# Performance work log

Hardware: AMD Instinct MI355X
Metric: run time of the kernel (lower is better)

Reference implementation:

```python
import jax, jax.numpy as jnp
import numpy as np

EPS = 1e-3  # Keras LayerNormalization default epsilon


def setup_inputs() -> dict:
    key = jax.random.key(0)
    ks = jax.random.split(key, 10)
    B, S, D, U = 4, 4096, 1024, 1024
    sc_in = 1.0 / np.sqrt(D)
    sc_u = 1.0 / np.sqrt(U)
    return {
        "inputs": jax.random.normal(ks[0], (B, S, D), dtype=jnp.float32),
        "w1": jax.random.normal(ks[1], (D, U), dtype=jnp.float32) * sc_in,
        "b1": jnp.zeros((U,), dtype=jnp.float32),
        "w2": jax.random.normal(ks[2], (U, U), dtype=jnp.float32) * sc_u,
        "b2": jnp.zeros((U,), dtype=jnp.float32),
        "wg": jax.random.normal(ks[3], (D, U), dtype=jnp.float32) * sc_in,
        "bg": jnp.zeros((U,), dtype=jnp.float32),
        "ws": jax.random.normal(ks[4], (D, U), dtype=jnp.float32) * sc_in,
        "bs": jnp.zeros((U,), dtype=jnp.float32),
        "gamma": jnp.ones((U,), dtype=jnp.float32),
        "beta": jnp.zeros((U,), dtype=jnp.float32),
    }


def reference(inputs, w1, b1, w2, b2, wg, bg, ws, bs, gamma, beta):
    # hidden branch: Dense(relu) -> (dropout inactive at inference) -> Dense
    h = jax.nn.relu(jnp.einsum('bsd,du->bsu', inputs, w1) + b1)
    x = jnp.einsum('bsu,uv->bsv', h, w2) + b2
    # gate on raw inputs
    g = jax.nn.sigmoid(jnp.einsum('bsd,du->bsu', inputs, wg) + bg)
    # skip projection
    s = jnp.einsum('bsd,du->bsu', inputs, ws) + bs
    y = x * g + s
    # LayerNormalization over last axis (Keras default eps=1e-3)
    mu = jnp.mean(y, axis=-1, keepdims=True)
    var = jnp.mean(jnp.square(y - mu), axis=-1, keepdims=True)
    return (y - mu) * jax.lax.rsqrt(var + EPS) * gamma + beta
```

## Files before the change

kernel.cpp:

```cpp
#include <hip/hip_runtime.h>
#include <hip/hip_bf16.h>

typedef short short8 __attribute__((ext_vector_type(8)));
typedef float f32x4 __attribute__((ext_vector_type(4)));

#define M_TOT 16384
#define NDIM  1024
#define BM 256
#define BN 256
#define BK 32
#define NT (NDIM / BK)

static __device__ __forceinline__ unsigned short f2bf(float f) {
  unsigned int u = __builtin_bit_cast(unsigned int, f);
  unsigned int r = (u + 0x7fffu + ((u >> 16) & 1u)) >> 16;
  return (unsigned short)r;
}
static __device__ __forceinline__ float bf2f(unsigned short u) {
  return __builtin_bit_cast(float, ((unsigned int)u) << 16);
}

#define CLB() asm volatile("" ::: "memory")

__global__ __launch_bounds__(256) void cast_in(const float* __restrict__ in,
                                               unsigned short* __restrict__ out,
                                               int n4) {
  int i = blockIdx.x * 256 + threadIdx.x;
  if (i >= n4) return;
  float4 v = reinterpret_cast<const float4*>(in)[i];
  ushort4 o;
  o.x = f2bf(v.x); o.y = f2bf(v.y); o.z = f2bf(v.z); o.w = f2bf(v.w);
  reinterpret_cast<ushort4*>(out)[i] = o;
}

__global__ __launch_bounds__(256) void tcast(const float* __restrict__ src,
                                             unsigned short* __restrict__ dst) {
  __shared__ unsigned short tile[32][33];
  int bx = blockIdx.x * 32, by = blockIdx.y * 32;
  int x = threadIdx.x & 31, y = threadIdx.x >> 5;
#pragma unroll
  for (int i = 0; i < 32; i += 8)
    tile[y + i][x] = f2bf(src[(size_t)(by + y + i) * NDIM + bx + x]);
  __syncthreads();
#pragma unroll
  for (int i = 0; i < 32; i += 8)
    dst[(size_t)(bx + y + i) * NDIM + by + x] = tile[x][y + i];
}

template <int MODE>
__global__ __launch_bounds__(512, 2) void gemm256(
    const unsigned short* __restrict__ A,
    const unsigned short* __restrict__ Bt,
    const float* __restrict__ bias,
    unsigned short* __restrict__ O,
    const unsigned short* __restrict__ G,
    const unsigned short* __restrict__ S) {
  __shared__ __align__(16) unsigned short lds[4][2][256][BK];

  const int tid = threadIdx.x;
  const int lane = tid & 63;
  const int wave = tid >> 6;
  const int wm = wave >> 2;
  const int wn = wave & 3;

  const int id = blockIdx.x;
  const int xcd = id & 7;
  const int slot0 = id >> 3;
  const int rblk = xcd + 8 * (slot0 >> 2);
  const int cblk = slot0 & 3;
  const int m0 = rblk * BM, n0 = cblk * BN;

  const unsigned short* gA = A + (size_t)m0 * NDIM;
  const unsigned short* gB = Bt + (size_t)n0 * NDIM;

  f32x4 acc[8][4] = {};

  auto stage = [&](int slot, int kt) {
#pragma unroll
    for (int q = 0; q < 4; ++q) {
      int cid = q * 512 + tid;
      int mat = q >> 1;
      int local = cid & 1023;
      int row = local >> 2;
      int c = (local & 3) ^ ((row >> 1) & 3);
      const unsigned short* g =
          (mat ? gB : gA) + (size_t)row * NDIM + kt * BK + c * 8;
      unsigned short* l = &lds[slot][mat][0][0] +
                          (size_t)((q * 512 + (tid & ~63)) & 1023) * 8;
      __builtin_amdgcn_global_load_lds(
          (__attribute__((address_space(1))) void*)g,
          (__attribute__((address_space(3))) void*)l, 16, 0, 0);
    }
  };

  auto compute = [&](int slot) {
    short8 af[8], bf[4];
#pragma unroll
    for (int nj = 0; nj < 4; ++nj) {
      int row = wn * 64 + nj * 16 + (lane & 15);
      int cs = (lane >> 4) ^ ((row >> 1) & 3);
      bf[nj] = *reinterpret_cast<const short8*>(&lds[slot][1][row][cs * 8]);
    }
#pragma unroll
    for (int mi = 0; mi < 8; ++mi) {
      int row = wm * 128 + mi * 16 + (lane & 15);
      int cs = (lane >> 4) ^ ((row >> 1) & 3);
      af[mi] = *reinterpret_cast<const short8*>(&lds[slot][0][row][cs * 8]);
    }
    __builtin_amdgcn_s_setprio(1);
#pragma unroll
    for (int mi = 0; mi < 8; ++mi)
#pragma unroll
      for (int nj = 0; nj < 4; ++nj)
        acc[mi][nj] = __builtin_amdgcn_mfma_f32_16x16x32_bf16(
            af[mi], bf[nj], acc[mi][nj], 0, 0, 0);
    __builtin_amdgcn_s_setprio(0);
  };

#define VMW(N) asm volatile("s_waitcnt vmcnt(" #N ")" ::: "memory")
#define BAR() do { CLB(); __builtin_amdgcn_s_barrier(); CLB(); } while (0)

  stage(0, 0);
  stage(1, 1);
  stage(2, 2);
  VMW(8);
  BAR();

#pragma unroll 4
  for (int t = 0; t < NT - 4; ++t) {
    stage((t + 3) & 3, t + 3);
    compute(t & 3);
    VMW(8);
    BAR();
  }
  stage(3, 31);
  compute(0);
  VMW(8);
  BAR();
  compute(1);
  VMW(4);
  BAR();
  compute(2);
  VMW(0);
  BAR();
  compute(3);

  const int crow0 = m0 + wm * 128;
  const int ccol0 = n0 + wn * 64;
#pragma unroll
  for (int mi = 0; mi < 8; ++mi) {
#pragma unroll
    for (int nj = 0; nj < 4; ++nj) {
      int row = crow0 + mi * 16 + ((lane >> 4) << 2);
      int col = ccol0 + nj * 16 + (lane & 15);
      float bc = bias[col];
#pragma unroll
      for (int r = 0; r < 4; ++r) {
        float v = acc[mi][nj][r] + bc;
        size_t idx = (size_t)(row + r) * NDIM + col;
        if (MODE == 0) {
          O[idx] = f2bf(fmaxf(v, 0.f));
        } else if (MODE == 1) {
          O[idx] = f2bf(1.f / (1.f + __expf(-v)));
        } else if (MODE == 2) {
          O[idx] = f2bf(v);
        } else {
          O[idx] = f2bf(v * bf2f(G[idx]) + bf2f(S[idx]));
        }
      }
    }
  }
#undef VMW
#undef BAR
}

__global__ __launch_bounds__(256) void layernorm_bf(
    const unsigned short* __restrict__ Ybf, float* __restrict__ Out,
    const float* __restrict__ gamma, const float* __restrict__ beta) {
  const int tid = threadIdx.x;
  const unsigned short* y = Ybf + (size_t)blockIdx.x * NDIM;
  ushort4 u = reinterpret_cast<const ushort4*>(y)[tid];
  float v0 = bf2f(u.x), v1 = bf2f(u.y), v2 = bf2f(u.z), v3 = bf2f(u.w);
  float s1 = v0 + v1 + v2 + v3;
  float s2 = v0 * v0 + v1 * v1 + v2 * v2 + v3 * v3;
#pragma unroll
  for (int o = 32; o > 0; o >>= 1) {
    s1 += __shfl_down(s1, o, 64);
    s2 += __shfl_down(s2, o, 64);
  }
  __shared__ float red[8];
  int wave = tid >> 6, lane = tid & 63;
  if (lane == 0) { red[wave] = s1; red[wave + 4] = s2; }
  __syncthreads();
  float S1 = red[0] + red[1] + red[2] + red[3];
  float S2 = red[4] + red[5] + red[6] + red[7];
  float mu = S1 * (1.f / NDIM);
  float var = S2 * (1.f / NDIM) - mu * mu;
  float inv = rsqrtf(var + 1e-3f);
  float4 gm = reinterpret_cast<const float4*>(gamma)[tid];
  float4 bt = reinterpret_cast<const float4*>(beta)[tid];
  float4 o;
  o.x = (v0 - mu) * inv * gm.x + bt.x;
  o.y = (v1 - mu) * inv * gm.y + bt.y;
  o.z = (v2 - mu) * inv * gm.z + bt.z;
  o.w = (v3 - mu) * inv * gm.w + bt.w;
  reinterpret_cast<float4*>(Out + (size_t)blockIdx.x * NDIM)[tid] = o;
}

extern "C" void kernel_launch(void* const* d_in, const int* in_sizes, int n_in,
                              void* d_out, int out_size, void* d_ws, size_t ws_size,
                              hipStream_t stream) {
  const float* inp = (const float*)d_in[0];
  const float* w1 = (const float*)d_in[1];
  const float* b1 = (const float*)d_in[2];
  const float* w2 = (const float*)d_in[3];
  const float* b2 = (const float*)d_in[4];
  const float* wg = (const float*)d_in[5];
  const float* bg = (const float*)d_in[6];
  const float* wsk = (const float*)d_in[7];
  const float* bs = (const float*)d_in[8];
  const float* gamma = (const float*)d_in[9];
  const float* beta = (const float*)d_in[10];

  char* p = (char*)d_ws;
  const size_t act_bf16 = (size_t)M_TOT * NDIM * 2;
  const size_t w_bf16 = (size_t)NDIM * NDIM * 2;
  unsigned short* Ain = (unsigned short*)p; p += act_bf16;
  unsigned short* H   = (unsigned short*)p; p += act_bf16;
  unsigned short* G   = (unsigned short*)p; p += act_bf16;
  unsigned short* S   = (unsigned short*)p; p += act_bf16;
  unsigned short* Ybf = (unsigned short*)p; p += act_bf16;
  unsigned short* W1t = (unsigned short*)p; p += w_bf16;
  unsigned short* W2t = (unsigned short*)p; p += w_bf16;
  unsigned short* Wgt = (unsigned short*)p; p += w_bf16;
  unsigned short* Wst = (unsigned short*)p; p += w_bf16;

  cast_in<<<(M_TOT * NDIM / 4 + 255) / 256, 256, 0, stream>>>(inp, Ain, M_TOT * NDIM / 4);
  dim3 tg(32, 32);
  tcast<<<tg, 256, 0, stream>>>(w1, W1t);
  tcast<<<tg, 256, 0, stream>>>(w2, W2t);
  tcast<<<tg, 256, 0, stream>>>(wg, Wgt);
  tcast<<<tg, 256, 0, stream>>>(wsk, Wst);

  const int nblk = (M_TOT / BM) * (NDIM / BN);
  gemm256<0><<<nblk, 512, 0, stream>>>(Ain, W1t, b1, H, nullptr, nullptr);
  gemm256<1><<<nblk, 512, 0, stream>>>(Ain, Wgt, bg, G, nullptr, nullptr);
  gemm256<2><<<nblk, 512, 0, stream>>>(Ain, Wst, bs, S, nullptr, nullptr);
  gemm256<3><<<nblk, 512, 0, stream>>>(H, W2t, b2, Ybf, G, S);
  layernorm_bf<<<M_TOT, 256, 0, stream>>>(Ybf, (float*)d_out, gamma, beta);
}
```

Measured before the change: 201.6 us.

## Fuse the three input-projection GEMMs into one kernel sharing the A tile

Replaces three separate GEMM launches over the input (W1, gate, skip) with one kernel. Each 128x128 block loads the A tile once and multiplies it against all three weight tiles, writing relu, sigmoid and linear outputs from the epilogue. This cuts repeated loads of the input activations and two kernel launches. In exchange it uses a simpler double-buffered pipeline with two barriers per step, smaller tiles, and 192 accumulator registers per thread, which raises register pressure.

```diff
diff --git a/kernel.cpp b/kernel.cpp
--- a/kernel.cpp
+++ b/kernel.cpp
@@ -6,8 +6,6 @@
 
 #define M_TOT 16384
 #define NDIM  1024
-#define BM 256
-#define BN 256
 #define BK 32
 #define NT (NDIM / BK)
 
@@ -21,6 +19,8 @@
 }
 
 #define CLB() asm volatile("" ::: "memory")
+#define VMW(N) asm volatile("s_waitcnt vmcnt(" #N ")" ::: "memory")
+#define BAR() do { CLB(); __builtin_amdgcn_s_barrier(); CLB(); } while (0)
 
 __global__ __launch_bounds__(256) void cast_in(const float* __restrict__ in,
                                                unsigned short* __restrict__ out,
@@ -47,8 +47,123 @@
     dst[(size_t)(bx + y + i) * NDIM + by + x] = tile[x][y + i];
 }
 
-template <int MODE>
-__global__ __launch_bounds__(512, 2) void gemm256(
+__global__ __launch_bounds__(256, 2) void trigemm(
+    const unsigned short* __restrict__ A,
+    const unsigned short* __restrict__ W1t,
+    const unsigned short* __restrict__ Wgt,
+    const unsigned short* __restrict__ Wst,
+    const float* __restrict__ b1,
+    const float* __restrict__ bg,
+    const float* __restrict__ bs,
+    unsigned short* __restrict__ H,
+    unsigned short* __restrict__ G,
+    unsigned short* __restrict__ S) {
+  __shared__ __align__(16) unsigned short lds[2][4][128][BK];
+
+  const int tid = threadIdx.x;
+  const int lane = tid & 63;
+  const int wave = tid >> 6;
+  const int wm = wave >> 1;
+  const int wn = wave & 1;
+
+  const int id = blockIdx.x;
+  const int xcd = id & 7;
+  const int slot = id >> 3;
+  const int rblk = xcd + 8 * (slot >> 3);
+  const int cblk = slot & 7;
+  const int m0 = rblk * 128, n0 = cblk * 128;
+
+  const unsigned short* gA = A + (size_t)m0 * NDIM;
+  const unsigned short* gW[3] = {W1t + (size_t)n0 * NDIM, Wgt + (size_t)n0 * NDIM,
+                                 Wst + (size_t)n0 * NDIM};
+
+  f32x4 acc[3][4][4] = {};
+
+  auto stage = [&](int buf, int kt) {
+#pragma unroll
+    for (int q = 0; q < 8; ++q) {
+      const int mat = q >> 1;
+      int local = (q & 1) * 256 + tid;
+      int row = local >> 2;
+      int c = (local & 3) ^ ((row >> 1) & 3);
+      const unsigned short* g =
+          (mat == 0 ? gA : gW[mat - 1]) + (size_t)row * NDIM + kt * BK + c * 8;
+      unsigned short* l = &lds[buf][0][0][0] +
+                          (size_t)(q * 256 + (tid & ~63)) * 8;
+      __builtin_amdgcn_global_load_lds(
+          (__attribute__((address_space(1))) void*)g,
+          (__attribute__((address_space(3))) void*)l, 16, 0, 0);
+    }
+  };
+
+  auto compute = [&](int buf) {
+    short8 af[4];
+#pragma unroll
+    for (int mi = 0; mi < 4; ++mi) {
+      int row = wm * 64 + mi * 16 + (lane & 15);
+      int cs = (lane >> 4) ^ ((row >> 1) & 3);
+      af[mi] = *reinterpret_cast<const short8*>(&lds[buf][0][row][cs * 8]);
+    }
+#pragma unroll
+    for (int w = 0; w < 3; ++w) {
+      short8 bf[4];
+#pragma unroll
+      for (int nj = 0; nj < 4; ++nj) {
+        int row = wn * 64 + nj * 16 + (lane & 15);
+        int cs = (lane >> 4) ^ ((row >> 1) & 3);
+        bf[nj] = *reinterpret_cast<const short8*>(&lds[buf][1 + w][row][cs * 8]);
+      }
+      __builtin_amdgcn_s_setprio(1);
+#pragma unroll
+      for (int mi = 0; mi < 4; ++mi)
+#pragma unroll
+        for (int nj = 0; nj < 4; ++nj)
+          acc[w][mi][nj] = __builtin_amdgcn_mfma_f32_16x16x32_bf16(
+              af[mi], bf[nj], acc[w][mi][nj], 0, 0, 0);
+      __builtin_amdgcn_s_setprio(0);
+    }
+  };
+
+  stage(0, 0);
+  for (int t = 0; t < NT; ++t) {
+    const int cur = t & 1;
+    if (t + 1 < NT) {
+      stage(cur ^ 1, t + 1);
+      VMW(8);
+    } else {
+      VMW(0);
+    }
+    BAR();
+    compute(cur);
+    BAR();
+  }
+
+  const int crow0 = m0 + wm * 64;
+  const int ccol0 = n0 + wn * 64;
+#pragma unroll
+  for (int w = 0; w < 3; ++w) {
+    const float* bptr = (w == 0) ? b1 : (w == 1) ? bg : bs;
+    unsigned short* optr = (w == 0) ? H : (w == 1) ? G : S;
+#pragma unroll
+    for (int mi = 0; mi < 4; ++mi) {
+#pragma unroll
+      for (int nj = 0; nj < 4; ++nj) {
+        int row = crow0 + mi * 16 + ((lane >> 4) << 2);
+        int col = ccol0 + nj * 16 + (lane & 15);
+        float bc = bptr[col];
+#pragma unroll
+        for (int r = 0; r < 4; ++r) {
+          float v = acc[w][mi][nj][r] + bc;
+          if (w == 0) v = fmaxf(v, 0.f);
+          else if (w == 1) v = 1.f / (1.f + __expf(-v));
+          optr[(size_t)(row + r) * NDIM + col] = f2bf(v);
+        }
+      }
+    }
+  }
+}
+
+__global__ __launch_bounds__(512, 2) void gemm_y(
     const unsigned short* __restrict__ A,
     const unsigned short* __restrict__ Bt,
     const float* __restrict__ bias,
@@ -68,7 +183,7 @@
   const int slot0 = id >> 3;
   const int rblk = xcd + 8 * (slot0 >> 2);
   const int cblk = slot0 & 3;
-  const int m0 = rblk * BM, n0 = cblk * BN;
+  const int m0 = rblk * 256, n0 = cblk * 256;
 
   const unsigned short* gA = A + (size_t)m0 * NDIM;
   const unsigned short* gB = Bt + (size_t)n0 * NDIM;
@@ -117,9 +232,6 @@
     __builtin_amdgcn_s_setprio(0);
   };
 
-#define VMW(N) asm volatile("s_waitcnt vmcnt(" #N ")" ::: "memory")
-#define BAR() do { CLB(); __builtin_amdgcn_s_barrier(); CLB(); } while (0)
-
   stage(0, 0);
   stage(1, 1);
   stage(2, 2);
@@ -158,20 +270,10 @@
       for (int r = 0; r < 4; ++r) {
         float v = acc[mi][nj][r] + bc;
         size_t idx = (size_t)(row + r) * NDIM + col;
-        if (MODE == 0) {
-          O[idx] = f2bf(fmaxf(v, 0.f));
-        } else if (MODE == 1) {
-          O[idx] = f2bf(1.f / (1.f + __expf(-v)));
-        } else if (MODE == 2) {
-          O[idx] = f2bf(v);
-        } else {
-          O[idx] = f2bf(v * bf2f(G[idx]) + bf2f(S[idx]));
-        }
+        O[idx] = f2bf(v * bf2f(G[idx]) + bf2f(S[idx]));
       }
     }
   }
-#undef VMW
-#undef BAR
 }
 
 __global__ __launch_bounds__(256) void layernorm_bf(
@@ -242,10 +344,8 @@
   tcast<<<tg, 256, 0, stream>>>(wg, Wgt);
   tcast<<<tg, 256, 0, stream>>>(wsk, Wst);
 
-  const int nblk = (M_TOT / BM) * (NDIM / BN);
-  gemm256<0><<<nblk, 512, 0, stream>>>(Ain, W1t, b1, H, nullptr, nullptr);
-  gemm256<1><<<nblk, 512, 0, stream>>>(Ain, Wgt, bg, G, nullptr, nullptr);
-  gemm256<2><<<nblk, 512, 0, stream>>>(Ain, Wst, bs, S, nullptr, nullptr);
-  gemm256<3><<<nblk, 512, 0, stream>>>(H, W2t, b2, Ybf, G, S);
+  trigemm<<<(M_TOT / 128) * (NDIM / 128), 256, 0, stream>>>(
+      Ain, W1t, Wgt, Wst, b1, bg, bs, H, G, S);
+  gemm_y<<<(M_TOT / 256) * (NDIM / 256), 512, 0, stream>>>(H, W2t, b2, Ybf, G, S);
   layernorm_bf<<<M_TOT, 256, 0, stream>>>(Ybf, (float*)d_out, gamma, beta);
 }
```

New measurement: 195.2 us. -3.2%, faster.

## Restructure GEMM into 8-phase ping-pong pipeline with BK=64 half-tile staging

Applied to the files above, without the earlier changes.

Replaces the 4-slot BK=32 GEMM main loop with a double-buffered BK=64 scheme. Each tile is split into 128-row halves that are staged one at a time, interleaved with quarter-tile MFMA blocks across eight barrier-separated phases. LDS swizzling changes to an 8-chunk XOR pattern. The four weight transpose-cast launches are also merged into one kernel with a z-dimension. The goal is finer overlap of global-to-LDS loads with MFMA work and fewer loop iterations, at the cost of many more barriers per iteration.

```diff
diff --git a/kernel.cpp b/kernel.cpp
--- a/kernel.cpp
+++ b/kernel.cpp
@@ -6,10 +6,8 @@
 
 #define M_TOT 16384
 #define NDIM  1024
-#define BM 256
-#define BN 256
-#define BK 32
-#define NT (NDIM / BK)
+#define BK 64
+#define NI (NDIM / (2 * BK))
 
 static __device__ __forceinline__ unsigned short f2bf(float f) {
   unsigned int u = __builtin_bit_cast(unsigned int, f);
@@ -21,6 +19,9 @@
 }
 
 #define CLB() asm volatile("" ::: "memory")
+#define VMW(N) asm volatile("s_waitcnt vmcnt(" #N ")" ::: "memory")
+#define LGKM0() asm volatile("s_waitcnt lgkmcnt(0)" ::: "memory")
+#define BAR() do { CLB(); __builtin_amdgcn_s_barrier(); CLB(); } while (0)
 
 __global__ __launch_bounds__(256) void cast_in(const float* __restrict__ in,
                                                unsigned short* __restrict__ out,
@@ -33,8 +34,14 @@
   reinterpret_cast<ushort4*>(out)[i] = o;
 }
 
-__global__ __launch_bounds__(256) void tcast(const float* __restrict__ src,
-                                             unsigned short* __restrict__ dst) {
+__global__ __launch_bounds__(256) void tcast4(
+    const float* __restrict__ w1, const float* __restrict__ w2,
+    const float* __restrict__ wg, const float* __restrict__ ws,
+    unsigned short* __restrict__ W1t, unsigned short* __restrict__ W2t,
+    unsigned short* __restrict__ Wgt, unsigned short* __restrict__ Wst) {
+  const int z = blockIdx.z;
+  const float* src = (z == 0) ? w1 : (z == 1) ? w2 : (z == 2) ? wg : ws;
+  unsigned short* dst = (z == 0) ? W1t : (z == 1) ? W2t : (z == 2) ? Wgt : Wst;
   __shared__ unsigned short tile[32][33];
   int bx = blockIdx.x * 32, by = blockIdx.y * 32;
   int x = threadIdx.x & 31, y = threadIdx.x >> 5;
@@ -48,102 +55,152 @@
 }
 
 template <int MODE>
-__global__ __launch_bounds__(512, 2) void gemm256(
+__global__ __launch_bounds__(512, 2) void gemm8p(
     const unsigned short* __restrict__ A,
     const unsigned short* __restrict__ Bt,
     const float* __restrict__ bias,
     unsigned short* __restrict__ O,
     const unsigned short* __restrict__ G,
     const unsigned short* __restrict__ S) {
-  __shared__ __align__(16) unsigned short lds[4][2][256][BK];
+  __shared__ __align__(16) unsigned short lds[2][2][2][128][64];
 
   const int tid = threadIdx.x;
   const int lane = tid & 63;
   const int wave = tid >> 6;
   const int wm = wave >> 2;
   const int wn = wave & 3;
+  const int lr = lane & 15;
+  const int lk = lane >> 4;
 
   const int id = blockIdx.x;
   const int xcd = id & 7;
-  const int slot0 = id >> 3;
-  const int rblk = xcd + 8 * (slot0 >> 2);
-  const int cblk = slot0 & 3;
-  const int m0 = rblk * BM, n0 = cblk * BN;
+  const int slot = id >> 3;
+  const int rblk = xcd + 8 * (slot >> 2);
+  const int cblk = slot & 3;
+  const int m0 = rblk * 256, n0 = cblk * 256;
 
   const unsigned short* gA = A + (size_t)m0 * NDIM;
   const unsigned short* gB = Bt + (size_t)n0 * NDIM;
 
   f32x4 acc[8][4] = {};
 
-  auto stage = [&](int slot, int kt) {
-#pragma unroll
-    for (int q = 0; q < 4; ++q) {
-      int cid = q * 512 + tid;
-      int mat = q >> 1;
-      int local = cid & 1023;
-      int row = local >> 2;
-      int c = (local & 3) ^ ((row >> 1) & 3);
-      const unsigned short* g =
-          (mat ? gB : gA) + (size_t)row * NDIM + kt * BK + c * 8;
-      unsigned short* l = &lds[slot][mat][0][0] +
-                          (size_t)((q * 512 + (tid & ~63)) & 1023) * 8;
+  auto stage = [&](int s, int mat, int h, int kt) {
+    const unsigned short* gb =
+        (mat ? gB : gA) + (size_t)(h * 128) * NDIM + kt * BK;
+    unsigned short* lb = &lds[s][mat][h][0][0];
+#pragma unroll
+    for (int q = 0; q < 2; ++q) {
+      int c = q * 512 + tid;
+      int row = c >> 3;
+      int kc = (c & 7) ^ (row & 7);
+      const unsigned short* g = gb + (size_t)row * NDIM + kc * 8;
+      unsigned short* l = lb + (size_t)(q * 512 + (tid & ~63)) * 8;
       __builtin_amdgcn_global_load_lds(
           (__attribute__((address_space(1))) void*)g,
           (__attribute__((address_space(3))) void*)l, 16, 0, 0);
     }
   };
 
-  auto compute = [&](int slot) {
-    short8 af[8], bf[4];
-#pragma unroll
-    for (int nj = 0; nj < 4; ++nj) {
-      int row = wn * 64 + nj * 16 + (lane & 15);
-      int cs = (lane >> 4) ^ ((row >> 1) & 3);
-      bf[nj] = *reinterpret_cast<const short8*>(&lds[slot][1][row][cs * 8]);
-    }
-#pragma unroll
-    for (int mi = 0; mi < 8; ++mi) {
-      int row = wm * 128 + mi * 16 + (lane & 15);
-      int cs = (lane >> 4) ^ ((row >> 1) & 3);
-      af[mi] = *reinterpret_cast<const short8*>(&lds[slot][0][row][cs * 8]);
-    }
-    __builtin_amdgcn_s_setprio(1);
-#pragma unroll
-    for (int mi = 0; mi < 8; ++mi)
-#pragma unroll
-      for (int nj = 0; nj < 4; ++nj)
-        acc[mi][nj] = __builtin_amdgcn_mfma_f32_16x16x32_bf16(
-            af[mi], bf[nj], acc[mi][nj], 0, 0, 0);
-    __builtin_amdgcn_s_setprio(0);
+  auto ldA = [&](short8* d, int s, int mih) {
+#pragma unroll
+    for (int mi = 0; mi < 4; ++mi)
+#pragma unroll
+      for (int kk = 0; kk < 2; ++kk) {
+        int lrow = (mih * 4 + mi) * 16 + lr;
+        int kc = (kk * 4 + lk) ^ (lr & 7);
+        d[mi * 2 + kk] =
+            *reinterpret_cast<const short8*>(&lds[s][0][wm][lrow][kc * 8]);
+      }
   };
-
-#define VMW(N) asm volatile("s_waitcnt vmcnt(" #N ")" ::: "memory")
-#define BAR() do { CLB(); __builtin_amdgcn_s_barrier(); CLB(); } while (0)
-
-  stage(0, 0);
-  stage(1, 1);
-  stage(2, 2);
-  VMW(8);
-  BAR();
-
-#pragma unroll 4
-  for (int t = 0; t < NT - 4; ++t) {
-    stage((t + 3) & 3, t + 3);
-    compute(t & 3);
-    VMW(8);
-    BAR();
-  }
-  stage(3, 31);
-  compute(0);
-  VMW(8);
-  BAR();
-  compute(1);
+  auto ldB = [&](short8* d, int s, int njh) {
+#pragma unroll
+    for (int nj = 0; nj < 2; ++nj)
+#pragma unroll
+      for (int kk = 0; kk < 2; ++kk) {
+        int lrow = (wn & 1) * 64 + (njh * 2 + nj) * 16 + lr;
+        int kc = (kk * 4 + lk) ^ (lr & 7);
+        d[nj * 2 + kk] = *reinterpret_cast<const short8*>(
+            &lds[s][1][wn >> 1][lrow][kc * 8]);
+      }
+  };
+
+#define QUAD(AF, BF, MI0, NJ0)                                              \
+  do {                                                                     \
+    __builtin_amdgcn_s_setprio(1);                                         \
+    _Pragma("unroll") for (int kk = 0; kk < 2; ++kk)                       \
+    _Pragma("unroll") for (int mi = 0; mi < 4; ++mi)                       \
+    _Pragma("unroll") for (int nj = 0; nj < 2; ++nj)                       \
+      acc[MI0 + mi][NJ0 + nj] = __builtin_amdgcn_mfma_f32_16x16x32_bf16(   \
+          AF[mi * 2 + kk], BF[nj * 2 + kk], acc[MI0 + mi][NJ0 + nj], 0, 0, 0); \
+    __builtin_amdgcn_s_setprio(0);                                         \
+  } while (0)
+
+  stage(0, 1, 0, 0);
+  stage(0, 1, 1, 0);
+  stage(0, 0, 0, 0);
+  stage(0, 0, 1, 0);
+  stage(1, 1, 0, 1);
+  stage(1, 1, 1, 1);
   VMW(4);
   BAR();
-  compute(2);
-  VMW(0);
-  BAR();
-  compute(3);
+
+  short8 aF[8], b01[4], b23[4];
+
+  for (int t = 0; t < NI; ++t) {
+    const bool more = (t + 1 < NI);
+    const int te = 2 * t + 2;
+    const int to = 2 * t + 3;
+
+    stage(1, 0, 0, 2 * t + 1);
+    ldA(aF, 0, 0);
+    ldB(b01, 0, 0);
+    BAR(); LGKM0();
+    QUAD(aF, b01, 0, 0);
+    BAR();
+
+    stage(1, 0, 1, 2 * t + 1);
+    ldB(b23, 0, 1);
+    BAR(); LGKM0();
+    QUAD(aF, b23, 0, 2);
+    BAR();
+
+    if (more) stage(0, 1, 0, te);
+    ldA(aF, 0, 1);
+    BAR(); LGKM0();
+    QUAD(aF, b23, 4, 2);
+    BAR();
+
+    if (more) stage(0, 1, 1, te);
+    BAR();
+    QUAD(aF, b01, 4, 0);
+    if (more) { VMW(4); } else { VMW(0); }
+    BAR();
+
+    if (more) stage(0, 0, 0, te);
+    ldA(aF, 1, 0);
+    ldB(b01, 1, 0);
+    BAR(); LGKM0();
+    QUAD(aF, b01, 0, 0);
+    BAR();
+
+    if (more) stage(0, 0, 1, te);
+    ldB(b23, 1, 1);
+    BAR(); LGKM0();
+    QUAD(aF, b23, 0, 2);
+    BAR();
+
+    if (more) stage(1, 1, 0, to);
+    ldA(aF, 1, 1);
+    BAR(); LGKM0();
+    QUAD(aF, b23, 4, 2);
+    BAR();
+
+    if (more) stage(1, 1, 1, to);
+    BAR();
+    QUAD(aF, b01, 4, 0);
+    if (more) VMW(4);
+    BAR();
+  }
 
   const int crow0 = m0 + wm * 128;
   const int ccol0 = n0 + wn * 64;
@@ -151,8 +208,8 @@
   for (int mi = 0; mi < 8; ++mi) {
 #pragma unroll
     for (int nj = 0; nj < 4; ++nj) {
-      int row = crow0 + mi * 16 + ((lane >> 4) << 2);
-      int col = ccol0 + nj * 16 + (lane & 15);
+      int row = crow0 + mi * 16 + (lk << 2);
+      int col = ccol0 + nj * 16 + lr;
       float bc = bias[col];
 #pragma unroll
       for (int r = 0; r < 4; ++r) {
@@ -170,8 +227,7 @@
       }
     }
   }
-#undef VMW
-#undef BAR
+#undef QUAD
 }
 
 __global__ __launch_bounds__(256) void layernorm_bf(
@@ -236,16 +292,12 @@
   unsigned short* Wst = (unsigned short*)p; p += w_bf16;
 
   cast_in<<<(M_TOT * NDIM / 4 + 255) / 256, 256, 0, stream>>>(inp, Ain, M_TOT * NDIM / 4);
-  dim3 tg(32, 32);
-  tcast<<<tg, 256, 0, stream>>>(w1, W1t);
-  tcast<<<tg, 256, 0, stream>>>(w2, W2t);
-  tcast<<<tg, 256, 0, stream>>>(wg, Wgt);
-  tcast<<<tg, 256, 0, stream>>>(wsk, Wst);
-
-  const int nblk = (M_TOT / BM) * (NDIM / BN);
-  gemm256<0><<<nblk, 512, 0, stream>>>(Ain, W1t, b1, H, nullptr, nullptr);
-  gemm256<1><<<nblk, 512, 0, stream>>>(Ain, Wgt, bg, G, nullptr, nullptr);
-  gemm256<2><<<nblk, 512, 0, stream>>>(Ain, Wst, bs, S, nullptr, nullptr);
-  gemm256<3><<<nblk, 512, 0, stream>>>(H, W2t, b2, Ybf, G, S);
+  tcast4<<<dim3(32, 32, 4), 256, 0, stream>>>(w1, w2, wg, wsk, W1t, W2t, Wgt, Wst);
+
+  const int nblk = (M_TOT / 256) * (NDIM / 256);
+  gemm8p<0><<<nblk, 512, 0, stream>>>(Ain, W1t, b1, H, nullptr, nullptr);
+  gemm8p<1><<<nblk, 512, 0, stream>>>(Ain, Wgt, bg, G, nullptr, nullptr);
+  gemm8p<2><<<nblk, 512, 0, stream>>>(Ain, Wst, bs, S, nullptr, nullptr);
+  gemm8p<3><<<nblk, 512, 0, stream>>>(H, W2t, b2, Ybf, G, S);
   layernorm_bf<<<M_TOT, 256, 0, stream>>>(Ybf, (float*)d_out, gamma, beta);
 }
```

Measured after the change: 218.9 us. +8.6%, slower.
